# Optimization experiments

Hardware: AMD Instinct MI355X
Metric: run time of the kernel (lower is better)

Reference implementation:

```python
import jax, jax.numpy as jnp
import numpy as np
from jax import lax

N = 100000
E = 1600000
LAG = 50
H = 32          # hid_dim = in_channels = out_channels
FEA = 4
OUT = 1


def setup_inputs() -> dict:
    key = jax.random.key(0)
    ks = jax.random.split(key, 16)
    inp = {
        "node_x": jax.random.normal(ks[0], (N, FEA), jnp.float32),
        "node_yx": jax.random.normal(ks[1], (N, LAG), jnp.float32),
        "edge_index": jax.random.randint(ks[2], (2, E), 0, N, jnp.int64),
        "edge_weight": jax.random.uniform(ks[3], (E,), jnp.float32),
        # LSTM params (torch gate order: i, f, g, o)
        "w_ih": jax.random.normal(ks[4], (4 * H, 1), jnp.float32) * 0.1,
        "w_hh": jax.random.normal(ks[5], (4 * H, H), jnp.float32) * 0.1,
        "b_ih": jnp.zeros((4 * H,), jnp.float32),
        "b_hh": jnp.zeros((4 * H,), jnp.float32),
        # time attention
        "att_W": jax.random.normal(ks[6], (LAG, H), jnp.float32) * 0.1,
        # fc after attention pooling
        "fc_W": jax.random.normal(ks[7], (H, H), jnp.float32) * 0.1,
        "fc_b": jnp.zeros((H,), jnp.float32),
        # GCN layers
        "gcn1_W": jax.random.normal(ks[8], (H, H), jnp.float32) * 0.1,
        "gcn1_b": jnp.zeros((H,), jnp.float32),
        "gcn2_W": jax.random.normal(ks[9], (H, H), jnp.float32) * 0.1,
        "gcn2_b": jnp.zeros((H,), jnp.float32),
        # final linear
        "lin_W": jax.random.normal(ks[10], (H + FEA, OUT), jnp.float32) * 0.1,
        "lin_b": jnp.zeros((OUT,), jnp.float32),
    }
    return inp


def _lstm(x, w_ih, w_hh, b_ih, b_hh):
    # x: [N, T, in_dim]; returns ht: [N, T, H]
    n, t, _ = x.shape
    h = w_hh.shape[1]
    xp = jnp.einsum('nti,gi->ntg', x, w_ih) + b_ih  # [N,T,4H], precompute input proj
    xp = jnp.swapaxes(xp, 0, 1)                      # [T,N,4H]

    def step(carry, xt):
        hprev, cprev = carry
        g = xt + hprev @ w_hh.T + b_hh               # [N,4H]
        i = jax.nn.sigmoid(g[:, 0 * h:1 * h])
        f = jax.nn.sigmoid(g[:, 1 * h:2 * h])
        gg = jnp.tanh(g[:, 2 * h:3 * h])
        o = jax.nn.sigmoid(g[:, 3 * h:4 * h])
        c = f * cprev + i * gg
        hnew = o * jnp.tanh(c)
        return (hnew, c), hnew

    init = (jnp.zeros((n, h), x.dtype), jnp.zeros((n, h), x.dtype))
    _, hs = lax.scan(step, init, xp)
    return jnp.swapaxes(hs, 0, 1)                    # [N,T,H]


def _gcn(x, edge_index, edge_weight, W, b, num_nodes):
    # PyG GCNConv: x' = D^-1/2 (A + I) D^-1/2 (x W) + b
    xw = x @ W
    src = jnp.concatenate([edge_index[0], jnp.arange(num_nodes, dtype=edge_index.dtype)])
    dst = jnp.concatenate([edge_index[1], jnp.arange(num_nodes, dtype=edge_index.dtype)])
    ew = jnp.concatenate([edge_weight, jnp.ones((num_nodes,), edge_weight.dtype)])
    deg = jax.ops.segment_sum(ew, dst, num_segments=num_nodes)
    dis = jnp.where(deg > 0, deg ** -0.5, 0.0)
    norm = dis[src] * ew * dis[dst]                  # [E+N]
    msg = norm[:, None] * xw[src]                    # gather + scale
    out = jax.ops.segment_sum(msg, dst, num_segments=num_nodes)  # scatter-add
    return out + b


def reference(node_x, node_yx, edge_index, edge_weight,
              w_ih, w_hh, b_ih, b_hh, att_W, fc_W, fc_b,
              gcn1_W, gcn1_b, gcn2_W, gcn2_b, lin_W, lin_b):
    # ATT_LSTM
    ht = _lstm(node_yx[:, :, None], w_ih, w_hh, b_ih, b_hh)   # [N,LAG,H]
    scores = jnp.sum(ht * att_W, axis=2)                      # [N,LAG]
    att = jax.nn.softmax(scores, axis=1)
    pooled = jnp.einsum('nt,nth->nh', att, ht)                # [N,H]
    x1 = jax.nn.relu(pooled @ fc_W + fc_b)                    # [N,H]
    # dropout treated as identity (deterministic reference / eval mode)
    x2 = _gcn(x1, edge_index, edge_weight, gcn1_W, gcn1_b, N)
    x2 = _gcn(x2, edge_index, edge_weight, gcn2_W, gcn2_b, N)
    xcom = jnp.concatenate([x2, node_x], axis=1)              # [N,H+FEA]
    pred = jax.nn.relu(xcom @ lin_W + lin_b)                  # [N,1]
    return pred.squeeze(-1)                                   # [N]
```

## Files before the change

kernel.cpp:

```cpp
#include <hip/hip_runtime.h>
#include <math.h>

#define H 32
#define LAGN 50

typedef float f32x4 __attribute__((ext_vector_type(4)));
typedef short bf16x8 __attribute__((ext_vector_type(8)));

__device__ __forceinline__ float rcp_(float x){ return __builtin_amdgcn_rcpf(x); }
__device__ __forceinline__ float sigmoidf_(float x){ return rcp_(1.0f + __expf(-x)); }
__device__ __forceinline__ float tanhf_(float x){ return 1.0f - 2.0f*rcp_(__expf(2.0f*x) + 1.0f); }

__device__ __forceinline__ unsigned short bfhi(float f){
  unsigned u = __float_as_uint(f);
  return (unsigned short)((u + 0x7FFFu + ((u>>16)&1u)) >> 16);
}
__device__ __forceinline__ float bf2f(unsigned short h){
  return __uint_as_float(((unsigned)h)<<16);
}

__global__ __launch_bounds__(64, 2) void k_lstm(
    const float* __restrict__ yx,
    const float* __restrict__ w_ih,
    const float* __restrict__ w_hh,
    const float* __restrict__ b_ih,
    const float* __restrict__ b_hh,
    const float* __restrict__ att_W,
    const float* __restrict__ fc_W,
    const float* __restrict__ fc_b,
    float* __restrict__ x1,
    int N)
{
  __shared__ float hs[16*36];
  const int l  = threadIdx.x;
  const int q  = l >> 4;
  const int cl = l & 15;
  const int nb = blockIdx.x * 16;

  bf16x8 Bhi[8], Blo[8];
  #pragma unroll
  for (int T=0; T<8; ++T){
    const float* p = w_hh + (size_t)(16*T + cl)*H + 8*q;
    f32x4 w0 = *(const f32x4*)p;
    f32x4 w1 = *(const f32x4*)(p+4);
    #pragma unroll
    for (int i=0;i<4;i++){
      unsigned short hh0 = bfhi(w0[i]);
      Bhi[T][i]   = (short)hh0;  Blo[T][i]   = (short)bfhi(w0[i] - bf2f(hh0));
      unsigned short hh1 = bfhi(w1[i]);
      Bhi[T][4+i] = (short)hh1;  Blo[T][4+i] = (short)bfhi(w1[i] - bf2f(hh1));
    }
  }

  float wihv[8], bsv[8];
  #pragma unroll
  for (int T=0;T<8;T++){
    int colg = 16*T + cl;
    wihv[T] = w_ih[colg];
    bsv[T]  = b_ih[colg] + b_hh[colg];
  }

  #pragma unroll
  for (int i=l; i<16*36; i+=64) hs[i] = 0.f;

  float cst[4][2], Sv[4][2], mv[4], Zv[4];
  #pragma unroll
  for (int idx=0;idx<4;idx++){
    mv[idx] = -1e30f; Zv[idx] = 0.f;
    cst[idx][0]=0.f; cst[idx][1]=0.f; Sv[idx][0]=0.f; Sv[idx][1]=0.f;
  }

  float xtc[4], atc[2];
  #pragma unroll
  for (int idx=0;idx<4;idx++){
    int r = nb + 4*q + idx; if (r >= N) r = N-1;
    xtc[idx] = yx[(size_t)r*LAGN];
  }
  atc[0] = att_W[cl];  atc[1] = att_W[cl+16];

  #pragma unroll 1
  for (int t=0;t<LAGN;t++){
    int tn = (t+1<LAGN) ? t+1 : t;
    float xtn[4], atn[2];
    #pragma unroll
    for (int idx=0;idx<4;idx++){
      int r = nb + 4*q + idx; if (r >= N) r = N-1;
      xtn[idx] = yx[(size_t)r*LAGN + tn];
    }
    atn[0] = att_W[tn*H + cl];  atn[1] = att_W[tn*H + cl + 16];

    f32x4 a0 = *(const f32x4*)&hs[36*cl + 8*q];
    f32x4 a1 = *(const f32x4*)&hs[36*cl + 8*q + 4];
    bf16x8 Ahi, Alo;
    #pragma unroll
    for (int i=0;i<4;i++){
      unsigned short h0 = bfhi(a0[i]);
      Ahi[i]   = (short)h0;  Alo[i]   = (short)bfhi(a0[i] - bf2f(h0));
      unsigned short h1 = bfhi(a1[i]);
      Ahi[4+i] = (short)h1;  Alo[4+i] = (short)bfhi(a1[i] - bf2f(h1));
    }

    f32x4 C[8];
    #pragma unroll
    for (int T=0;T<8;T++){
      f32x4 z = {0.f,0.f,0.f,0.f};
      z = __builtin_amdgcn_mfma_f32_16x16x32_bf16(Ahi, Blo[T], z, 0,0,0);
      z = __builtin_amdgcn_mfma_f32_16x16x32_bf16(Alo, Bhi[T], z, 0,0,0);
      z = __builtin_amdgcn_mfma_f32_16x16x32_bf16(Ahi, Bhi[T], z, 0,0,0);
      C[T] = z;
    }

    float stp[4];
    float hv[4][2];
    #pragma unroll
    for (int idx=0; idx<4; ++idx){
      stp[idx] = 0.f;
      #pragma unroll
      for (int jh=0; jh<2; ++jh){
        float gi = C[jh][idx]   + xtc[idx]*wihv[jh]   + bsv[jh];
        float gf = C[2+jh][idx] + xtc[idx]*wihv[2+jh] + bsv[2+jh];
        float gg = C[4+jh][idx] + xtc[idx]*wihv[4+jh] + bsv[4+jh];
        float go = C[6+jh][idx] + xtc[idx]*wihv[6+jh] + bsv[6+jh];
        float iv = sigmoidf_(gi), fv = sigmoidf_(gf);
        float gv = tanhf_(gg),    ov = sigmoidf_(go);
        float cn = fv*cst[idx][jh] + iv*gv;
        cst[idx][jh] = cn;
        float hh = ov*tanhf_(cn);
        hv[idx][jh] = hh;
        stp[idx] += hh * atc[jh];
        hs[36*(4*q+idx) + cl + 16*jh] = hh;
      }
    }

    #pragma unroll
    for (int mask=1; mask<16; mask<<=1){
      #pragma unroll
      for (int idx=0;idx<4;idx++)
        stp[idx] += __shfl_xor(stp[idx], mask);
    }

    #pragma unroll
    for (int idx=0;idx<4;idx++){
      float mn = fmaxf(mv[idx], stp[idx]);
      float sc = __expf(mv[idx] - mn);
      float p  = __expf(stp[idx] - mn);
      Zv[idx] = Zv[idx]*sc + p;
      Sv[idx][0] = Sv[idx][0]*sc + p*hv[idx][0];
      Sv[idx][1] = Sv[idx][1]*sc + p*hv[idx][1];
      mv[idx] = mn;
    }
    #pragma unroll
    for (int idx=0;idx<4;idx++) xtc[idx] = xtn[idx];
    atc[0] = atn[0]; atc[1] = atn[1];
  }

  #pragma unroll
  for (int idx=0;idx<4;idx++){
    float iz = rcp_(Zv[idx]);
    hs[36*(4*q+idx) + cl]      = Sv[idx][0]*iz;
    hs[36*(4*q+idx) + cl + 16] = Sv[idx][1]*iz;
  }
  f32x4 p0 = *(const f32x4*)&hs[36*cl + 8*q];
  f32x4 p1 = *(const f32x4*)&hs[36*cl + 8*q + 4];
  bf16x8 Phi, Plo;
  #pragma unroll
  for (int i=0;i<4;i++){
    unsigned short h0 = bfhi(p0[i]);
    Phi[i]   = (short)h0;  Plo[i]   = (short)bfhi(p0[i] - bf2f(h0));
    unsigned short h1 = bfhi(p1[i]);
    Phi[4+i] = (short)h1;  Plo[4+i] = (short)bfhi(p1[i] - bf2f(h1));
  }

  #pragma unroll
  for (int T=0;T<2;T++){
    bf16x8 Fhi, Flo;
    #pragma unroll
    for (int i=0;i<8;i++){
      float wf = fc_W[(size_t)(8*q+i)*H + 16*T + cl];
      unsigned short hh = bfhi(wf);
      Fhi[i] = (short)hh; Flo[i] = (short)bfhi(wf - bf2f(hh));
    }
    float fcbv = fc_b[16*T + cl];
    f32x4 z = {0.f,0.f,0.f,0.f};
    z = __builtin_amdgcn_mfma_f32_16x16x32_bf16(Phi, Flo, z, 0,0,0);
    z = __builtin_amdgcn_mfma_f32_16x16x32_bf16(Plo, Fhi, z, 0,0,0);
    z = __builtin_amdgcn_mfma_f32_16x16x32_bf16(Phi, Fhi, z, 0,0,0);
    #pragma unroll
    for (int idx=0;idx<4;idx++){
      int r = nb + 4*q + idx;
      if (r < N) x1[(size_t)r*H + 16*T + cl] = fmaxf(z[idx] + fcbv, 0.f);
    }
  }
}

__global__ void k_deg_init(float* __restrict__ deg, int* __restrict__ cnt, int N){
  int i = blockIdx.x*blockDim.x + threadIdx.x;
  if (i < N){ deg[i] = 1.0f; cnt[i] = 0; }
}

__global__ void k_deg_cnt(const int* __restrict__ ei, const float* __restrict__ ew,
                          float* __restrict__ deg, int* __restrict__ cnt, int E){
  int e = blockIdx.x*blockDim.x + threadIdx.x;
  if (e < E){
    int d = ei[E+e];
    atomicAdd(&deg[d], ew[e]);
    atomicAdd(&cnt[d], 1);
  }
}

__global__ void k_dis(float* __restrict__ deg, int N){
  int i = blockIdx.x*blockDim.x + threadIdx.x;
  if (i < N) deg[i] = __frcp_rn(sqrtf(deg[i]));
}

__global__ __launch_bounds__(1024) void k_scan(const int* __restrict__ cnt,
                                               int* __restrict__ rowptr,
                                               int* __restrict__ pos, int N){
  __shared__ int wsum[16];
  __shared__ int carry;
  const int tid = threadIdx.x, lane = tid & 63, w = tid >> 6;
  if (tid == 0) carry = 0;
  __syncthreads();
  for (int base = 0; base < N; base += 1024){
    int i = base + tid;
    int v = (i < N) ? cnt[i] : 0;
    int s = v;
    #pragma unroll
    for (int off=1; off<64; off<<=1){
      int t = __shfl_up(s, off);
      if (lane >= off) s += t;
    }
    if (lane == 63) wsum[w] = s;
    __syncthreads();
    int woff = 0, tot = 0;
    #pragma unroll
    for (int k=0;k<16;k++){ int x = wsum[k]; tot += x; if (k < w) woff += x; }
    int excl = carry + woff + s - v;
    if (i < N){ rowptr[i] = excl; pos[i] = excl; }
    __syncthreads();
    if (tid == 0) carry += tot;
    __syncthreads();
  }
  if (tid == 0) rowptr[N] = carry;
}

__global__ void k_fill(const int* __restrict__ ei, const float* __restrict__ ew,
                       const float* __restrict__ dis, int* __restrict__ pos,
                       int* __restrict__ csrc, float* __restrict__ cnrm, int E){
  int e = blockIdx.x*blockDim.x + threadIdx.x;
  if (e < E){
    int s = ei[e], d = ei[E+e];
    int slot = atomicAdd(&pos[d], 1);
    csrc[slot] = s;
    cnrm[slot] = dis[s]*ew[e]*dis[d];
  }
}

__global__ __launch_bounds__(256) void k_xw(
    const float* __restrict__ x, const float* __restrict__ W,
    const float* __restrict__ b, const float* __restrict__ dis,
    float* __restrict__ xw, float* __restrict__ out, int N)
{
  int n = blockIdx.x*blockDim.x + threadIdx.x;
  if (n >= N) return;
  float xv[H];
  const float4* xr = (const float4*)(x + (size_t)n*H);
  #pragma unroll
  for (int q=0;q<H/4;q++){
    float4 v = xr[q];
    xv[4*q+0]=v.x; xv[4*q+1]=v.y; xv[4*q+2]=v.z; xv[4*q+3]=v.w;
  }
  float d = dis[n];
  float sn = d*d;
  float* xwr = xw + (size_t)n*H;
  float* outr = out + (size_t)n*H;
  #pragma unroll
  for (int j=0;j<H;j++){
    float a = 0.f;
    #pragma unroll
    for (int k=0;k<H;k++) a += xv[k]*W[k*H+j];
    xwr[j]  = a;
    outr[j] = sn*a + b[j];
  }
}

__global__ __launch_bounds__(256) void k_gather(
    const int* __restrict__ rowptr, const int* __restrict__ csrc,
    const float* __restrict__ cnrm, const float* __restrict__ xw,
    float* __restrict__ out, int N)
{
  int wid = (int)((blockIdx.x*256u + threadIdx.x) >> 6);
  if (wid >= N) return;
  int lane = threadIdx.x & 63;
  int ch = lane & 31;
  int eh = lane >> 5;
  int start = rowptr[wid], end = rowptr[wid+1];
  float acc = 0.f;
  for (int j = start + eh; j < end; j += 2){
    int s = csrc[j];
    acc += cnrm[j] * xw[(size_t)s*H + ch];
  }
  acc += __shfl_xor(acc, 32);
  if (eh == 0){
    float* o = out + (size_t)wid*H + ch;
    *o += acc;
  }
}

__global__ void k_final(const float* __restrict__ x2, const float* __restrict__ nx,
                        const float* __restrict__ lw, const float* __restrict__ lb,
                        float* __restrict__ out, int N)
{
  int n = blockIdx.x*blockDim.x + threadIdx.x;
  if (n >= N) return;
  float a = lb[0];
  const float* xr = x2 + (size_t)n*H;
  #pragma unroll
  for (int j=0;j<H;j++) a += xr[j]*lw[j];
  const float* nr = nx + (size_t)n*4;
  #pragma unroll
  for (int f=0;f<4;f++) a += nr[f]*lw[H+f];
  out[n] = fmaxf(a, 0.f);
}

extern "C" void kernel_launch(void* const* d_in, const int* in_sizes, int n_in,
                              void* d_out, int out_size, void* d_ws, size_t ws_size,
                              hipStream_t stream) {
  const float* node_x   = (const float*)d_in[0];
  const float* node_yx  = (const float*)d_in[1];
  const int*   edge_idx = (const int*)  d_in[2];
  const float* edge_w   = (const float*)d_in[3];
  const float* w_ih     = (const float*)d_in[4];
  const float* w_hh     = (const float*)d_in[5];
  const float* b_ih     = (const float*)d_in[6];
  const float* b_hh     = (const float*)d_in[7];
  const float* att_W    = (const float*)d_in[8];
  const float* fc_W     = (const float*)d_in[9];
  const float* fc_b     = (const float*)d_in[10];
  const float* gcn1_W   = (const float*)d_in[11];
  const float* gcn1_b   = (const float*)d_in[12];
  const float* gcn2_W   = (const float*)d_in[13];
  const float* gcn2_b   = (const float*)d_in[14];
  const float* lin_W    = (const float*)d_in[15];
  const float* lin_b    = (const float*)d_in[16];
  float* out = (float*)d_out;

  int N = in_sizes[0] / 4;
  int E = in_sizes[3];

  float* ws = (float*)d_ws;
  float* x1     = ws;
  float* xw     = x1  + (size_t)N*H;
  float* o1     = xw  + (size_t)N*H;
  float* deg    = o1  + (size_t)N*H;
  int*   rowptr = (int*)(deg + N);
  int*   pos    = rowptr + (N+1);
  int*   csrc   = pos + N;
  float* cnrm   = (float*)(csrc + E);

  dim3 blk(256);
  int gN  = (N + 255) / 256;
  int gE  = (E + 255) / 256;
  int gL  = (N + 15) / 16;
  int gG  = (N + 3) / 4;

  k_lstm<<<gL, dim3(64), 0, stream>>>(node_yx, w_ih, w_hh, b_ih, b_hh,
                                      att_W, fc_W, fc_b, x1, N);
  k_deg_init<<<gN, blk, 0, stream>>>(deg, pos, N);
  k_deg_cnt <<<gE, blk, 0, stream>>>(edge_idx, edge_w, deg, pos, E);
  k_dis     <<<gN, blk, 0, stream>>>(deg, N);
  k_scan    <<<1, dim3(1024), 0, stream>>>(pos, rowptr, pos, N);
  k_fill    <<<gE, blk, 0, stream>>>(edge_idx, edge_w, deg, pos, csrc, cnrm, E);
  k_xw    <<<gN, blk, 0, stream>>>(x1, gcn1_W, gcn1_b, deg, xw, o1, N);
  k_gather<<<gG, blk, 0, stream>>>(rowptr, csrc, cnrm, xw, o1, N);
  k_xw    <<<gN, blk, 0, stream>>>(o1, gcn2_W, gcn2_b, deg, xw, x1, N);
  k_gather<<<gG, blk, 0, stream>>>(rowptr, csrc, cnrm, xw, x1, N);
  k_final<<<gN, blk, 0, stream>>>(x1, node_x, lin_W, lin_b, out, N);
}
```

Baseline: 900.8 us.

## Rework LSTM block shape, drop online softmax max, parallelize scan, pack CSR edges

The LSTM kernel now runs four waves per 256-thread block. It uses packed hardware bf16 conversion, folds the input projection and bias into the MFMA accumulator, and drops the running-max rescaling in the attention softmax. The single-block serial scan is replaced by a three-kernel multi-block scan, and CSR source and norm are packed into one int2 array so the gather needs a single load. Skipping the softmax max subtraction risks overflow if attention scores grow large.

```diff
diff --git a/kernel.cpp b/kernel.cpp
--- a/kernel.cpp
+++ b/kernel.cpp
@@ -1,4 +1,6 @@
 #include <hip/hip_runtime.h>
+#include <hip/hip_bf16.h>
+#include <stdint.h>
 #include <math.h>
 
 #define H 32
@@ -11,15 +13,30 @@
 __device__ __forceinline__ float sigmoidf_(float x){ return rcp_(1.0f + __expf(-x)); }
 __device__ __forceinline__ float tanhf_(float x){ return 1.0f - 2.0f*rcp_(__expf(2.0f*x) + 1.0f); }
 
-__device__ __forceinline__ unsigned short bfhi(float f){
-  unsigned u = __float_as_uint(f);
-  return (unsigned short)((u + 0x7FFFu + ((u>>16)&1u)) >> 16);
-}
-__device__ __forceinline__ float bf2f(unsigned short h){
-  return __uint_as_float(((unsigned)h)<<16);
-}
-
-__global__ __launch_bounds__(64, 2) void k_lstm(
+__device__ __forceinline__ unsigned pk_bf2(float f0, float f1){
+  union { __hip_bfloat162 b; unsigned u; } cv;
+  cv.b = __float22bfloat162_rn(make_float2(f0, f1));
+  return cv.u;
+}
+__device__ __forceinline__ void cvt8v(f32x4 a, f32x4 b, bf16x8& hi, bf16x8& lo){
+  union U { bf16x8 v; unsigned d[4]; } Hu, Lu;
+  #pragma unroll
+  for (int p=0;p<2;p++){
+    float f0=a[2*p], f1=a[2*p+1];
+    unsigned uh = pk_bf2(f0,f1);
+    float h0 = __uint_as_float(uh<<16);
+    float h1 = __uint_as_float(uh & 0xffff0000u);
+    Hu.d[p] = uh;  Lu.d[p] = pk_bf2(f0-h0, f1-h1);
+    float g0=b[2*p], g1=b[2*p+1];
+    unsigned ug = pk_bf2(g0,g1);
+    float k0 = __uint_as_float(ug<<16);
+    float k1 = __uint_as_float(ug & 0xffff0000u);
+    Hu.d[2+p] = ug;  Lu.d[2+p] = pk_bf2(g0-k0, g1-k1);
+  }
+  hi = Hu.v; lo = Lu.v;
+}
+
+__global__ __launch_bounds__(256, 2) void k_lstm(
     const float* __restrict__ yx,
     const float* __restrict__ w_ih,
     const float* __restrict__ w_hh,
@@ -31,11 +48,13 @@
     float* __restrict__ x1,
     int N)
 {
-  __shared__ float hs[16*36];
-  const int l  = threadIdx.x;
+  __shared__ float hs[4][16*36];
+  const int wv = threadIdx.x >> 6;
+  const int l  = threadIdx.x & 63;
   const int q  = l >> 4;
   const int cl = l & 15;
-  const int nb = blockIdx.x * 16;
+  const int nb = blockIdx.x*64 + wv*16;
+  float* HS = hs[wv];
 
   bf16x8 Bhi[8], Blo[8];
   #pragma unroll
@@ -43,13 +62,7 @@
     const float* p = w_hh + (size_t)(16*T + cl)*H + 8*q;
     f32x4 w0 = *(const f32x4*)p;
     f32x4 w1 = *(const f32x4*)(p+4);
-    #pragma unroll
-    for (int i=0;i<4;i++){
-      unsigned short hh0 = bfhi(w0[i]);
-      Bhi[T][i]   = (short)hh0;  Blo[T][i]   = (short)bfhi(w0[i] - bf2f(hh0));
-      unsigned short hh1 = bfhi(w1[i]);
-      Bhi[T][4+i] = (short)hh1;  Blo[T][4+i] = (short)bfhi(w1[i] - bf2f(hh1));
-    }
+    cvt8v(w0, w1, Bhi[T], Blo[T]);
   }
 
   float wihv[8], bsv[8];
@@ -60,75 +73,59 @@
     bsv[T]  = b_ih[colg] + b_hh[colg];
   }
 
-  #pragma unroll
-  for (int i=l; i<16*36; i+=64) hs[i] = 0.f;
-
-  float cst[4][2], Sv[4][2], mv[4], Zv[4];
+  for (int i=l; i<16*36; i+=64) HS[i] = 0.f;
+
+  float cst[4][2], Sv[4][2], Zv[4];
   #pragma unroll
   for (int idx=0;idx<4;idx++){
-    mv[idx] = -1e30f; Zv[idx] = 0.f;
-    cst[idx][0]=0.f; cst[idx][1]=0.f; Sv[idx][0]=0.f; Sv[idx][1]=0.f;
-  }
-
-  float xtc[4], atc[2];
-  #pragma unroll
-  for (int idx=0;idx<4;idx++){
-    int r = nb + 4*q + idx; if (r >= N) r = N-1;
-    xtc[idx] = yx[(size_t)r*LAGN];
-  }
-  atc[0] = att_W[cl];  atc[1] = att_W[cl+16];
+    Zv[idx]=0.f; cst[idx][0]=0.f; cst[idx][1]=0.f; Sv[idx][0]=0.f; Sv[idx][1]=0.f;
+  }
+
+  const int rr = nb + 4*q;
+  const float* yp0 = yx + (size_t)(rr+0<N?rr+0:N-1)*LAGN;
+  const float* yp1 = yx + (size_t)(rr+1<N?rr+1:N-1)*LAGN;
+  const float* yp2 = yx + (size_t)(rr+2<N?rr+2:N-1)*LAGN;
+  const float* yp3 = yx + (size_t)(rr+3<N?rr+3:N-1)*LAGN;
 
   #pragma unroll 1
   for (int t=0;t<LAGN;t++){
-    int tn = (t+1<LAGN) ? t+1 : t;
-    float xtn[4], atn[2];
-    #pragma unroll
-    for (int idx=0;idx<4;idx++){
-      int r = nb + 4*q + idx; if (r >= N) r = N-1;
-      xtn[idx] = yx[(size_t)r*LAGN + tn];
-    }
-    atn[0] = att_W[tn*H + cl];  atn[1] = att_W[tn*H + cl + 16];
-
-    f32x4 a0 = *(const f32x4*)&hs[36*cl + 8*q];
-    f32x4 a1 = *(const f32x4*)&hs[36*cl + 8*q + 4];
+    float xtv[4] = {yp0[t], yp1[t], yp2[t], yp3[t]};
+    float at0 = att_W[t*H + cl];
+    float at1 = att_W[t*H + cl + 16];
+
+    f32x4 a0 = *(const f32x4*)&HS[36*cl + 8*q];
+    f32x4 a1 = *(const f32x4*)&HS[36*cl + 8*q + 4];
     bf16x8 Ahi, Alo;
-    #pragma unroll
-    for (int i=0;i<4;i++){
-      unsigned short h0 = bfhi(a0[i]);
-      Ahi[i]   = (short)h0;  Alo[i]   = (short)bfhi(a0[i] - bf2f(h0));
-      unsigned short h1 = bfhi(a1[i]);
-      Ahi[4+i] = (short)h1;  Alo[4+i] = (short)bfhi(a1[i] - bf2f(h1));
-    }
+    cvt8v(a0, a1, Ahi, Alo);
 
     f32x4 C[8];
     #pragma unroll
     for (int T=0;T<8;T++){
-      f32x4 z = {0.f,0.f,0.f,0.f};
+      f32x4 z;
+      #pragma unroll
+      for (int idx=0;idx<4;idx++) z[idx] = __builtin_fmaf(xtv[idx], wihv[T], bsv[T]);
       z = __builtin_amdgcn_mfma_f32_16x16x32_bf16(Ahi, Blo[T], z, 0,0,0);
       z = __builtin_amdgcn_mfma_f32_16x16x32_bf16(Alo, Bhi[T], z, 0,0,0);
       z = __builtin_amdgcn_mfma_f32_16x16x32_bf16(Ahi, Bhi[T], z, 0,0,0);
       C[T] = z;
     }
 
-    float stp[4];
-    float hv[4][2];
+    float stp[4], hv[4][2];
     #pragma unroll
     for (int idx=0; idx<4; ++idx){
       stp[idx] = 0.f;
       #pragma unroll
       for (int jh=0; jh<2; ++jh){
-        float gi = C[jh][idx]   + xtc[idx]*wihv[jh]   + bsv[jh];
-        float gf = C[2+jh][idx] + xtc[idx]*wihv[2+jh] + bsv[2+jh];
-        float gg = C[4+jh][idx] + xtc[idx]*wihv[4+jh] + bsv[4+jh];
-        float go = C[6+jh][idx] + xtc[idx]*wihv[6+jh] + bsv[6+jh];
-        float iv = sigmoidf_(gi), fv = sigmoidf_(gf);
-        float gv = tanhf_(gg),    ov = sigmoidf_(go);
+        float iv = sigmoidf_(C[jh][idx]);
+        float fv = sigmoidf_(C[2+jh][idx]);
+        float gv = tanhf_(C[4+jh][idx]);
+        float ov = sigmoidf_(C[6+jh][idx]);
         float cn = fv*cst[idx][jh] + iv*gv;
         cst[idx][jh] = cn;
         float hh = ov*tanhf_(cn);
         hv[idx][jh] = hh;
-        stp[idx] += hh * atc[jh];
-        hs[36*(4*q+idx) + cl + 16*jh] = hh;
+        stp[idx] += hh * (jh ? at1 : at0);
+        HS[36*(4*q+idx) + cl + 16*jh] = hh;
       }
     }
 
@@ -141,54 +138,43 @@
 
     #pragma unroll
     for (int idx=0;idx<4;idx++){
-      float mn = fmaxf(mv[idx], stp[idx]);
-      float sc = __expf(mv[idx] - mn);
-      float p  = __expf(stp[idx] - mn);
-      Zv[idx] = Zv[idx]*sc + p;
-      Sv[idx][0] = Sv[idx][0]*sc + p*hv[idx][0];
-      Sv[idx][1] = Sv[idx][1]*sc + p*hv[idx][1];
-      mv[idx] = mn;
-    }
-    #pragma unroll
-    for (int idx=0;idx<4;idx++) xtc[idx] = xtn[idx];
-    atc[0] = atn[0]; atc[1] = atn[1];
+      float pex = __expf(stp[idx]);
+      Zv[idx] += pex;
+      Sv[idx][0] += pex*hv[idx][0];
+      Sv[idx][1] += pex*hv[idx][1];
+    }
   }
 
   #pragma unroll
   for (int idx=0;idx<4;idx++){
     float iz = rcp_(Zv[idx]);
-    hs[36*(4*q+idx) + cl]      = Sv[idx][0]*iz;
-    hs[36*(4*q+idx) + cl + 16] = Sv[idx][1]*iz;
-  }
-  f32x4 p0 = *(const f32x4*)&hs[36*cl + 8*q];
-  f32x4 p1 = *(const f32x4*)&hs[36*cl + 8*q + 4];
+    HS[36*(4*q+idx) + cl]      = Sv[idx][0]*iz;
+    HS[36*(4*q+idx) + cl + 16] = Sv[idx][1]*iz;
+  }
+  f32x4 p0 = *(const f32x4*)&HS[36*cl + 8*q];
+  f32x4 p1 = *(const f32x4*)&HS[36*cl + 8*q + 4];
   bf16x8 Phi, Plo;
-  #pragma unroll
-  for (int i=0;i<4;i++){
-    unsigned short h0 = bfhi(p0[i]);
-    Phi[i]   = (short)h0;  Plo[i]   = (short)bfhi(p0[i] - bf2f(h0));
-    unsigned short h1 = bfhi(p1[i]);
-    Phi[4+i] = (short)h1;  Plo[4+i] = (short)bfhi(p1[i] - bf2f(h1));
-  }
+  cvt8v(p0, p1, Phi, Plo);
 
   #pragma unroll
   for (int T=0;T<2;T++){
+    f32x4 w0, w1;
+    #pragma unroll
+    for (int i=0;i<4;i++){
+      w0[i] = fc_W[(size_t)(8*q+i)*H + 16*T + cl];
+      w1[i] = fc_W[(size_t)(8*q+4+i)*H + 16*T + cl];
+    }
     bf16x8 Fhi, Flo;
-    #pragma unroll
-    for (int i=0;i<8;i++){
-      float wf = fc_W[(size_t)(8*q+i)*H + 16*T + cl];
-      unsigned short hh = bfhi(wf);
-      Fhi[i] = (short)hh; Flo[i] = (short)bfhi(wf - bf2f(hh));
-    }
+    cvt8v(w0, w1, Fhi, Flo);
     float fcbv = fc_b[16*T + cl];
-    f32x4 z = {0.f,0.f,0.f,0.f};
+    f32x4 z = {fcbv, fcbv, fcbv, fcbv};
     z = __builtin_amdgcn_mfma_f32_16x16x32_bf16(Phi, Flo, z, 0,0,0);
     z = __builtin_amdgcn_mfma_f32_16x16x32_bf16(Plo, Fhi, z, 0,0,0);
     z = __builtin_amdgcn_mfma_f32_16x16x32_bf16(Phi, Fhi, z, 0,0,0);
     #pragma unroll
     for (int idx=0;idx<4;idx++){
       int r = nb + 4*q + idx;
-      if (r < N) x1[(size_t)r*H + 16*T + cl] = fmaxf(z[idx] + fcbv, 0.f);
+      if (r < N) x1[(size_t)r*H + 16*T + cl] = fmaxf(z[idx], 0.f);
     }
   }
 }
@@ -213,46 +199,70 @@
   if (i < N) deg[i] = __frcp_rn(sqrtf(deg[i]));
 }
 
-__global__ __launch_bounds__(1024) void k_scan(const int* __restrict__ cnt,
-                                               int* __restrict__ rowptr,
-                                               int* __restrict__ pos, int N){
-  __shared__ int wsum[16];
-  __shared__ int carry;
-  const int tid = threadIdx.x, lane = tid & 63, w = tid >> 6;
-  if (tid == 0) carry = 0;
+__global__ __launch_bounds__(256) void k_scan1(const int* __restrict__ cnt,
+                                               int* __restrict__ bsum, int N){
+  __shared__ int wsm[4];
+  int b = blockIdx.x, t = threadIdx.x;
+  int base = b*1024 + t*4;
+  int s = 0;
+  #pragma unroll
+  for (int i=0;i<4;i++) if (base+i < N) s += cnt[base+i];
+  #pragma unroll
+  for (int off=1; off<64; off<<=1) s += __shfl_xor(s, off);
+  if ((t&63) == 0) wsm[t>>6] = s;
   __syncthreads();
-  for (int base = 0; base < N; base += 1024){
-    int i = base + tid;
-    int v = (i < N) ? cnt[i] : 0;
+  if (t == 0) bsum[b] = wsm[0]+wsm[1]+wsm[2]+wsm[3];
+}
+
+__global__ __launch_bounds__(64) void k_scan2(int* __restrict__ bsum, int nb){
+  int lane = threadIdx.x;
+  int carry = 0;
+  for (int base=0; base<nb; base+=64){
+    int i = base + lane;
+    int v = (i<nb) ? bsum[i] : 0;
     int s = v;
     #pragma unroll
-    for (int off=1; off<64; off<<=1){
-      int t = __shfl_up(s, off);
-      if (lane >= off) s += t;
-    }
-    if (lane == 63) wsum[w] = s;
-    __syncthreads();
-    int woff = 0, tot = 0;
-    #pragma unroll
-    for (int k=0;k<16;k++){ int x = wsum[k]; tot += x; if (k < w) woff += x; }
-    int excl = carry + woff + s - v;
-    if (i < N){ rowptr[i] = excl; pos[i] = excl; }
-    __syncthreads();
-    if (tid == 0) carry += tot;
-    __syncthreads();
-  }
-  if (tid == 0) rowptr[N] = carry;
+    for (int off=1; off<64; off<<=1){ int tt=__shfl_up(s,off); if (lane>=off) s+=tt; }
+    if (i<nb) bsum[i] = carry + s - v;
+    carry += __shfl(s, 63);
+  }
+}
+
+__global__ __launch_bounds__(256) void k_scan3(int* cp,
+                                               const int* __restrict__ bsum,
+                                               int* __restrict__ rowptr, int N){
+  __shared__ int wsm[4];
+  int b = blockIdx.x, t = threadIdx.x, lane = t&63, w = t>>6;
+  int base = b*1024 + t*4;
+  int v[4];
+  #pragma unroll
+  for (int i=0;i<4;i++) v[i] = (base+i<N) ? cp[base+i] : 0;
+  int tsum = v[0]+v[1]+v[2]+v[3];
+  int s = tsum;
+  #pragma unroll
+  for (int off=1; off<64; off<<=1){ int tt=__shfl_up(s,off); if (lane>=off) s+=tt; }
+  if (lane==63) wsm[w] = s;
+  __syncthreads();
+  int woff = 0;
+  #pragma unroll
+  for (int k=0;k<4;k++) if (k<w) woff += wsm[k];
+  int e = bsum[b] + woff + (s - tsum);
+  #pragma unroll
+  for (int i=0;i<4;i++){
+    if (base+i < N){ rowptr[base+i] = e; cp[base+i] = e; }
+    if (base+i == N-1) rowptr[N] = e + v[i];
+    e += v[i];
+  }
 }
 
 __global__ void k_fill(const int* __restrict__ ei, const float* __restrict__ ew,
                        const float* __restrict__ dis, int* __restrict__ pos,
-                       int* __restrict__ csrc, float* __restrict__ cnrm, int E){
+                       int2* __restrict__ cedge, int E){
   int e = blockIdx.x*blockDim.x + threadIdx.x;
   if (e < E){
     int s = ei[e], d = ei[E+e];
     int slot = atomicAdd(&pos[d], 1);
-    csrc[slot] = s;
-    cnrm[slot] = dis[s]*ew[e]*dis[d];
+    cedge[slot] = make_int2(s, __float_as_int(dis[s]*ew[e]*dis[d]));
   }
 }
 
@@ -285,9 +295,8 @@
 }
 
 __global__ __launch_bounds__(256) void k_gather(
-    const int* __restrict__ rowptr, const int* __restrict__ csrc,
-    const float* __restrict__ cnrm, const float* __restrict__ xw,
-    float* __restrict__ out, int N)
+    const int* __restrict__ rowptr, const int2* __restrict__ cedge,
+    const float* __restrict__ xw, float* __restrict__ out, int N)
 {
   int wid = (int)((blockIdx.x*256u + threadIdx.x) >> 6);
   if (wid >= N) return;
@@ -297,8 +306,8 @@
   int start = rowptr[wid], end = rowptr[wid+1];
   float acc = 0.f;
   for (int j = start + eh; j < end; j += 2){
-    int s = csrc[j];
-    acc += cnrm[j] * xw[(size_t)s*H + ch];
+    int2 e = cedge[j];
+    acc += __int_as_float(e.y) * xw[(size_t)e.x*H + ch];
   }
   acc += __shfl_xor(acc, 32);
   if (eh == 0){
@@ -355,25 +364,29 @@
   float* deg    = o1  + (size_t)N*H;
   int*   rowptr = (int*)(deg + N);
   int*   pos    = rowptr + (N+1);
-  int*   csrc   = pos + N;
-  float* cnrm   = (float*)(csrc + E);
+  uintptr_t ca  = ((uintptr_t)(pos + N) + 7) & ~(uintptr_t)7;
+  int2*  cedge  = (int2*)ca;
+  int*   bsum   = (int*)(cedge + E);
 
   dim3 blk(256);
   int gN  = (N + 255) / 256;
   int gE  = (E + 255) / 256;
-  int gL  = (N + 15) / 16;
+  int gL  = (N + 63) / 64;
   int gG  = (N + 3) / 4;
-
-  k_lstm<<<gL, dim3(64), 0, stream>>>(node_yx, w_ih, w_hh, b_ih, b_hh,
-                                      att_W, fc_W, fc_b, x1, N);
+  int gS  = (N + 1023) / 1024;
+
+  k_lstm<<<gL, blk, 0, stream>>>(node_yx, w_ih, w_hh, b_ih, b_hh,
+                                 att_W, fc_W, fc_b, x1, N);
   k_deg_init<<<gN, blk, 0, stream>>>(deg, pos, N);
   k_deg_cnt <<<gE, blk, 0, stream>>>(edge_idx, edge_w, deg, pos, E);
   k_dis     <<<gN, blk, 0, stream>>>(deg, N);
-  k_scan    <<<1, dim3(1024), 0, stream>>>(pos, rowptr, pos, N);
-  k_fill    <<<gE, blk, 0, stream>>>(edge_idx, edge_w, deg, pos, csrc, cnrm, E);
+  k_scan1   <<<gS, blk, 0, stream>>>(pos, bsum, N);
+  k_scan2   <<<1, dim3(64), 0, stream>>>(bsum, gS);
+  k_scan3   <<<gS, blk, 0, stream>>>(pos, bsum, rowptr, N);
+  k_fill    <<<gE, blk, 0, stream>>>(edge_idx, edge_w, deg, pos, cedge, E);
   k_xw    <<<gN, blk, 0, stream>>>(x1, gcn1_W, gcn1_b, deg, xw, o1, N);
-  k_gather<<<gG, blk, 0, stream>>>(rowptr, csrc, cnrm, xw, o1, N);
+  k_gather<<<gG, blk, 0, stream>>>(rowptr, cedge, xw, o1, N);
   k_xw    <<<gN, blk, 0, stream>>>(o1, gcn2_W, gcn2_b, deg, xw, x1, N);
-  k_gather<<<gG, blk, 0, stream>>>(rowptr, csrc, cnrm, xw, x1, N);
+  k_gather<<<gG, blk, 0, stream>>>(rowptr, cedge, xw, x1, N);
   k_final<<<gN, blk, 0, stream>>>(x1, node_x, lin_W, lin_b, out, N);
 }
```

Measured after the change: 772.9 us. 1.17x faster.
